# Kernel tuning notes

Hardware: AMD Instinct MI355X
Metric: run time of the kernel (lower is better)

## Reference

```python
import jax, jax.numpy as jnp
import numpy as np

THRESH = 0.5
TAU = 0.5
GAMMA = 1.0  # ZIF surrogate-gradient width


@jax.custom_vjp
def zif(v):
    # Heaviside spike with rectangular surrogate gradient (ZIF)
    return (v > 0).astype(v.dtype)


def _zif_fwd(v):
    return zif(v), v


def _zif_bwd(v, g):
    # grad = clamp(gamma - |v|, min=0) / gamma^2
    tmp = jnp.clip(GAMMA - jnp.abs(v), 0.0) * (1.0 / (GAMMA * GAMMA))
    return (g * tmp,)


zif.defvjp(_zif_fwd, _zif_bwd)


def setup_inputs() -> dict:
    key = jax.random.key(0)
    x = jax.random.normal(key, (256, 1024, 128), dtype=jnp.float32)  # [B, C, T]
    return {"x": x}


def reference(x):
    # x: [B, C, T]; LIF scan over time axis with soft reset
    xt = jnp.moveaxis(x, 2, 0)  # [T, B, C]

    def step(mem, xi):
        mem = mem * TAU + xi
        spike = zif(mem - THRESH)
        mem = mem - spike * THRESH  # soft reset
        return mem, spike

    _, spikes = jax.lax.scan(step, jnp.zeros_like(xt[0]), xt)  # [T, B, C]
    return jnp.moveaxis(spikes, 0, 2)  # [B, C, T]
```

## Files before the change

kernel.cpp:

```cpp
#include <hip/hip_runtime.h>


#define TAU 0.5f
#define THRESH 0.5f
#define ROWS 256
#define T 128
#define CHUNK 32
#define PADF 36

__global__ __launch_bounds__(256) void lif_kernel(const float* __restrict__ x,
                                                  float* __restrict__ out) {
    __shared__ float lds[ROWS * PADF];
    const int tid = threadIdx.x;
    const long long blockBase = (long long)blockIdx.x * ROWS * T;

    float mem = 0.0f;
    for (int c0 = 0; c0 < T; c0 += CHUNK) {
#pragma unroll
        for (int t = 0; t < 8; ++t) {
            const int i = tid + t * 256;
            const int r = i >> 3;
            const int c = (i & 7) << 2;
            float4 v = *reinterpret_cast<const float4*>(
                x + blockBase + (long long)r * T + c0 + c);
            *reinterpret_cast<float4*>(&lds[r * PADF + c]) = v;
        }
        __syncthreads();

        float* myrow = &lds[tid * PADF];
#pragma unroll
        for (int j = 0; j < CHUNK / 4; ++j) {
            float4 v = *reinterpret_cast<float4*>(&myrow[j * 4]);
            float4 s;
            mem = mem * TAU + v.x; s.x = (mem > THRESH) ? 1.0f : 0.0f; mem -= s.x * THRESH;
            mem = mem * TAU + v.y; s.y = (mem > THRESH) ? 1.0f : 0.0f; mem -= s.y * THRESH;
            mem = mem * TAU + v.z; s.z = (mem > THRESH) ? 1.0f : 0.0f; mem -= s.z * THRESH;
            mem = mem * TAU + v.w; s.w = (mem > THRESH) ? 1.0f : 0.0f; mem -= s.w * THRESH;
            *reinterpret_cast<float4*>(&myrow[j * 4]) = s;
        }
        __syncthreads();

#pragma unroll
        for (int t = 0; t < 8; ++t) {
            const int i = tid + t * 256;
            const int r = i >> 3;
            const int c = (i & 7) << 2;
            float4 s = *reinterpret_cast<float4*>(&lds[r * PADF + c]);
            *reinterpret_cast<float4*>(out + blockBase + (long long)r * T + c0 + c) = s;
        }
        __syncthreads();
    }
}

extern "C" void kernel_launch(void* const* d_in, const int* in_sizes, int n_in,
                              void* d_out, int out_size, void* d_ws, size_t ws_size,
                              hipStream_t stream) {
    const float* x = (const float*)d_in[0];
    float* out = (float*)d_out;
    const int rows = out_size / T;
    const int grid = rows / ROWS;
    lif_kernel<<<grid, ROWS, 0, stream>>>(x, out);
}
```

Baseline: 45.74 us.

## Load inputs directly per row with prefetch, halve block size, nontemporal stores

Each thread now reads its own row's 32-element chunk straight from global memory into registers instead of staging coalesced loads through LDS. The next chunk is prefetched while the current spikes are written out. Block size drops to 128 rows, giving more blocks and higher occupancy, and output stores use nontemporal hints. Per-thread row loads are strided across lanes (512B apart), so load coalescing gets worse in exchange for removing an LDS round trip and one barrier.

```diff
diff --git a/kernel.cpp b/kernel.cpp
--- a/kernel.cpp
+++ b/kernel.cpp
@@ -3,52 +3,63 @@
 
 #define TAU 0.5f
 #define THRESH 0.5f
-#define ROWS 256
 #define T 128
+#define ROWS 128
 #define CHUNK 32
 #define PADF 36
 
-__global__ __launch_bounds__(256) void lif_kernel(const float* __restrict__ x,
-                                                  float* __restrict__ out) {
+typedef float floatx4 __attribute__((ext_vector_type(4)));
+
+__global__ __launch_bounds__(128, 4) void lif_kernel(const float* __restrict__ x,
+                                                     float* __restrict__ out) {
     __shared__ float lds[ROWS * PADF];
     const int tid = threadIdx.x;
     const long long blockBase = (long long)blockIdx.x * ROWS * T;
+    const floatx4* __restrict__ xin4 =
+        reinterpret_cast<const floatx4*>(x + blockBase + (long long)tid * T);
 
     float mem = 0.0f;
-    for (int c0 = 0; c0 < T; c0 += CHUNK) {
+    floatx4 v[8];
 #pragma unroll
-        for (int t = 0; t < 8; ++t) {
-            const int i = tid + t * 256;
-            const int r = i >> 3;
-            const int c = (i & 7) << 2;
-            float4 v = *reinterpret_cast<const float4*>(
-                x + blockBase + (long long)r * T + c0 + c);
-            *reinterpret_cast<float4*>(&lds[r * PADF + c]) = v;
+    for (int j = 0; j < 8; ++j) v[j] = xin4[j];
+
+#pragma unroll
+    for (int k = 0; k < 4; ++k) {
+        const int c0 = k * CHUNK;
+
+#pragma unroll
+        for (int j = 0; j < 8; ++j) {
+            floatx4 t = v[j];
+            floatx4 s;
+            mem = mem * TAU + t.x; s.x = (mem > THRESH) ? 1.0f : 0.0f; mem -= s.x * THRESH;
+            mem = mem * TAU + t.y; s.y = (mem > THRESH) ? 1.0f : 0.0f; mem -= s.y * THRESH;
+            mem = mem * TAU + t.z; s.z = (mem > THRESH) ? 1.0f : 0.0f; mem -= s.z * THRESH;
+            mem = mem * TAU + t.w; s.w = (mem > THRESH) ? 1.0f : 0.0f; mem -= s.w * THRESH;
+            *reinterpret_cast<floatx4*>(&lds[tid * PADF + j * 4]) = s;
         }
         __syncthreads();
 
-        float* myrow = &lds[tid * PADF];
+        floatx4 nv[8];
+        if (k < 3) {
 #pragma unroll
-        for (int j = 0; j < CHUNK / 4; ++j) {
-            float4 v = *reinterpret_cast<float4*>(&myrow[j * 4]);
-            float4 s;
-            mem = mem * TAU + v.x; s.x = (mem > THRESH) ? 1.0f : 0.0f; mem -= s.x * THRESH;
-            mem = mem * TAU + v.y; s.y = (mem > THRESH) ? 1.0f : 0.0f; mem -= s.y * THRESH;
-            mem = mem * TAU + v.z; s.z = (mem > THRESH) ? 1.0f : 0.0f; mem -= s.z * THRESH;
-            mem = mem * TAU + v.w; s.w = (mem > THRESH) ? 1.0f : 0.0f; mem -= s.w * THRESH;
-            *reinterpret_cast<float4*>(&myrow[j * 4]) = s;
+            for (int j = 0; j < 8; ++j) nv[j] = xin4[(k + 1) * 8 + j];
+        }
+
+#pragma unroll
+        for (int t = 0; t < 8; ++t) {
+            const int i = tid + t * ROWS;
+            const int r = i >> 3;
+            const int c = (i & 7) << 2;
+            floatx4 s = *reinterpret_cast<floatx4*>(&lds[r * PADF + c]);
+            __builtin_nontemporal_store(
+                s, reinterpret_cast<floatx4*>(out + blockBase + (long long)r * T + c0 + c));
         }
         __syncthreads();
 
+        if (k < 3) {
 #pragma unroll
-        for (int t = 0; t < 8; ++t) {
-            const int i = tid + t * 256;
-            const int r = i >> 3;
-            const int c = (i & 7) << 2;
-            float4 s = *reinterpret_cast<float4*>(&lds[r * PADF + c]);
-            *reinterpret_cast<float4*>(out + blockBase + (long long)r * T + c0 + c) = s;
+            for (int j = 0; j < 8; ++j) v[j] = nv[j];
         }
-        __syncthreads();
     }
 }
 
```

Result: no change. 45.13 us (-1.3%).
